# Optimization experiments

Hardware: AMD Instinct MI355X
Metric: run time of the kernel (lower is better)

## Reference

```python
import jax, jax.numpy as jnp
import numpy as np

N_TOKENS, E, H = 20000, 128, 512
B, T, L = 128, 512, 8


def setup_inputs() -> dict:
    key = jax.random.key(0)
    ks = jax.random.split(key, 9)
    s = 0.02
    return {
        "tokens": jax.random.randint(ks[0], (B, T, L), 0, N_TOKENS),
        "values": jax.random.uniform(ks[1], (B, T, L), dtype=jnp.float32),
        "emb": jax.random.normal(ks[2], (N_TOKENS, E), dtype=jnp.float32) * s,
        "W_ih": jax.random.normal(ks[3], (4 * H, E), dtype=jnp.float32) * s,
        "W_hh": jax.random.normal(ks[4], (4 * H, H), dtype=jnp.float32) * s,
        "b_ih": jnp.zeros((4 * H,), jnp.float32),
        "b_hh": jnp.zeros((4 * H,), jnp.float32),
        "W_out": jax.random.normal(ks[5], (1, H), dtype=jnp.float32) * s,
        "b_out": jnp.zeros((1,), jnp.float32),
    }


def reference(tokens, values, emb, W_ih, W_hh, b_ih, b_hh, W_out, b_out):
    # EmbedTimeseriesW: value-weighted sum of token embeddings per time bin
    e = emb[tokens]                                  # [B,T,L,E]
    x = jnp.einsum('btle,btl->bte', e, values)       # [B,T,E]
    x = jax.nn.relu(x)                               # ReLU (dropout p=0 -> identity)

    xT = jnp.swapaxes(x, 0, 1)                       # [T,B,E]
    b = b_ih + b_hh

    def step(carry, xt):
        h, c = carry
        gates = xt @ W_ih.T + h @ W_hh.T + b         # [B,4H]
        i, f, g, o = jnp.split(gates, 4, axis=-1)    # torch LSTM gate order
        c = jax.nn.sigmoid(f) * c + jax.nn.sigmoid(i) * jnp.tanh(g)
        h = jax.nn.sigmoid(o) * jnp.tanh(c)
        return (h, c), h

    h0 = jnp.zeros((x.shape[0], W_hh.shape[1]), x.dtype)
    (_, _), hs = jax.lax.scan(step, (h0, h0), xT)    # hs: [T,B,H]

    out = jnp.swapaxes(hs, 0, 1) @ W_out.T + b_out   # [B,T,1]
    return out.squeeze(-1)                           # [B,T]
```

## Files before the change

kernel.cpp:

```cpp
#include <hip/hip_runtime.h>
#include <hip/hip_bf16.h>

#define B_   128
#define T_   512
#define L_   8
#define E_   128
#define H_   512

#define NG_   8
#define WPG_  16
#define JW_   32
#define GSTR  132
#define HBUFB 131072
#define BARSA_OFF (3 * HBUFB)
#define FAST_BYTES (BARSA_OFF + NG_ * 64 * 4)
#define SPIN_MAX 4096

typedef __attribute__((ext_vector_type(8))) short s8v;
typedef __attribute__((ext_vector_type(4))) float f4v;
typedef __attribute__((ext_vector_type(4))) unsigned int u32x4;
typedef unsigned long long u64;
typedef unsigned int u32;

__device__ __forceinline__ float bf16u_to_f(unsigned short s) {
  union { unsigned u; float f; } c; c.u = ((unsigned)s) << 16; return c.f;
}
__device__ __forceinline__ u64 llc_load8(const void* p) {
  return __hip_atomic_load((const u64*)p, __ATOMIC_RELAXED, __HIP_MEMORY_SCOPE_AGENT);
}
__device__ __forceinline__ unsigned llc_load4(const unsigned* p) {
  return __hip_atomic_load(p, __ATOMIC_RELAXED, __HIP_MEMORY_SCOPE_AGENT);
}
__device__ __forceinline__ void llc_store4(unsigned* p, unsigned v) {
  __hip_atomic_store(p, v, __ATOMIC_RELAXED, __HIP_MEMORY_SCOPE_AGENT);
}
__device__ __forceinline__ float sigf(float x) {
  return __builtin_amdgcn_rcpf(1.f + __expf(-x));
}
__device__ __forceinline__ float tanh_f(float x) {
  return 1.f - 2.f * __builtin_amdgcn_rcpf(1.f + __expf(2.f * x));
}

__device__ __forceinline__ void buf_store_sc0(u32x4 srd, unsigned voff, unsigned v) {
  asm volatile("buffer_store_dword %0, %1, %2, 0 offen sc0"
               :: "v"(v), "v"(voff), "s"(srd) : "memory");
}
__device__ __forceinline__ unsigned buf_load_sc0(u32x4 srd, unsigned voff) {
  unsigned v;
  asm volatile("buffer_load_dword %0, %1, %2, 0 offen sc0\n\ts_waitcnt vmcnt(0)"
               : "=v"(v) : "v"(voff), "s"(srd) : "memory");
  return v;
}

__device__ __forceinline__ bool wait_flags_fast(u32x4 srd, unsigned polloff, unsigned tgt) {
  for (int it = 0; it < SPIN_MAX; ++it) {
    unsigned v = buf_load_sc0(srd, polloff);
    if (__all((int)(v >= tgt))) return true;
    __builtin_amdgcn_s_sleep(1);
  }
  return false;
}
__device__ __forceinline__ void wait_flags_slow(const u32* flags, unsigned tgt) {
  const u32* p = flags + (threadIdx.x & 63);
  while (!__all((int)(llc_load4(p) >= tgt))) __builtin_amdgcn_s_sleep(1);
}

__global__ void embed_kernel(const int* __restrict__ tokens,
                             const float* __restrict__ values,
                             const float* __restrict__ emb,
                             __hip_bfloat16* __restrict__ x_bf) {
  int idx = blockIdx.x * blockDim.x + threadIdx.x;
  int e  = idx & (E_ - 1);
  int bt = idx >> 7;
  int b  = bt >> 9;
  int t  = bt & (T_ - 1);
  const int*   tok = tokens + (size_t)bt * L_;
  const float* val = values + (size_t)bt * L_;
  float acc = 0.f;
#pragma unroll
  for (int l = 0; l < L_; ++l) acc += emb[(size_t)tok[l] * E_ + e] * val[l];
  acc = fmaxf(acc, 0.f);
  x_bf[((size_t)t * B_ + b) * E_ + e] = __float2bfloat16(acc);
}

__device__ __forceinline__ void fill_slab(u32x4* __restrict__ h_lds4, int mode,
                                          u32x4 srd, unsigned voffA,
                                          const u64* __restrict__ slow_src,
                                          int tid) {
  u32x4 c0, c1, c2, c3;
  if (mode == 0) {
    asm volatile(
        "buffer_load_dwordx4 %0, %4, %5, 0 offen sc0\n\t"
        "buffer_load_dwordx4 %1, %4, %5, 0 offen offset:16 sc0\n\t"
        "buffer_load_dwordx4 %2, %4, %5, 0 offen offset:32 sc0\n\t"
        "buffer_load_dwordx4 %3, %4, %5, 0 offen offset:48 sc0\n\t"
        "s_waitcnt vmcnt(0)"
        : "=&v"(c0), "=&v"(c1), "=&v"(c2), "=&v"(c3)
        : "v"(voffA), "s"(srd) : "memory");
  } else {
    u64 a, b;
    a = llc_load8(slow_src + 0); b = llc_load8(slow_src + 1);
    c0 = (u32x4){(u32)a, (u32)(a >> 32), (u32)b, (u32)(b >> 32)};
    a = llc_load8(slow_src + 2); b = llc_load8(slow_src + 3);
    c1 = (u32x4){(u32)a, (u32)(a >> 32), (u32)b, (u32)(b >> 32)};
    a = llc_load8(slow_src + 4); b = llc_load8(slow_src + 5);
    c2 = (u32x4){(u32)a, (u32)(a >> 32), (u32)b, (u32)(b >> 32)};
    a = llc_load8(slow_src + 6); b = llc_load8(slow_src + 7);
    c3 = (u32x4){(u32)a, (u32)(a >> 32), (u32)b, (u32)(b >> 32)};
  }
  const int row = tid >> 4;
  const int sw2 = row & 7;
  const int cb  = (tid & 15) * 4;
  u32x4* dst = h_lds4 + (size_t)row * 64;
  dst[(cb + 0) ^ sw2] = c0;
  dst[(cb + 1) ^ sw2] = c1;
  dst[(cb + 2) ^ sw2] = c2;
  dst[(cb + 3) ^ sw2] = c3;
}

__device__ __forceinline__ void out_dot_lds16(const u32x4* __restrict__ h_lds4,
                                              int t, int gid,
                                              const float* __restrict__ wout_s,
                                              float bout, float* __restrict__ out) {
  const int um = threadIdx.x >> 4;
  const int uj = threadIdx.x & 15;
  const u64* row = (const u64*)(h_lds4 + (size_t)um * 64);
  const float* wr = wout_s + uj * 32;
  float p = 0.f;
#pragma unroll
  for (int j = 0; j < 4; ++j) {
    int pc = ((uj * 4 + j) ^ (um & 7)) * 2;
    u64 qa = row[pc], qb = row[pc + 1];
    p += bf16u_to_f((unsigned short)(qa      )) * wr[j * 8 + 0];
    p += bf16u_to_f((unsigned short)(qa >> 16)) * wr[j * 8 + 1];
    p += bf16u_to_f((unsigned short)(qa >> 32)) * wr[j * 8 + 2];
    p += bf16u_to_f((unsigned short)(qa >> 48)) * wr[j * 8 + 3];
    p += bf16u_to_f((unsigned short)(qb      )) * wr[j * 8 + 4];
    p += bf16u_to_f((unsigned short)(qb >> 16)) * wr[j * 8 + 5];
    p += bf16u_to_f((unsigned short)(qb >> 32)) * wr[j * 8 + 6];
    p += bf16u_to_f((unsigned short)(qb >> 48)) * wr[j * 8 + 7];
  }
  p += __shfl_down(p, 8, 16);
  p += __shfl_down(p, 4, 16);
  p += __shfl_down(p, 2, 16);
  p += __shfl_down(p, 1, 16);
  if (uj == 0) out[(size_t)(gid * 16 + um) * T_ + t] = p + bout;
}

__global__ void __launch_bounds__(256, 1)
lstm_kernel(const float* __restrict__ W_ih, const float* __restrict__ W_hh,
            const float* __restrict__ b_ih, const float* __restrict__ b_hh,
            const float* __restrict__ W_out, const float* __restrict__ b_out,
            const __hip_bfloat16* __restrict__ x_bf,
            u64* __restrict__ h_slow,
            float* __restrict__ out,
            u32* __restrict__ barsB,
            u32* __restrict__ xcc_tab,
            char* __restrict__ fastbase) {
  __shared__ __align__(16) u32x4 h_lds4[16 * 64];
  __shared__ __align__(16) float gbuf[16][GSTR];
  __shared__ __align__(16) float bias_s[128];
  __shared__ float wout_s[H_];
  __shared__ int   cnt_same_s, bad_grp_s, mode_s;

  const int tid = threadIdx.x;
  const int wg  = blockIdx.x;
  const int gid = wg & (NG_ - 1);
  const int g   = wg >> 3;
  const int j0g = g * JW_;

  const int wv   = tid >> 6;
  const int lane = tid & 63;
  const int m16  = lane & 15;
  const int q    = lane >> 4;
  const int sw   = m16 & 7;

  u32x4 srd;
  {
    unsigned long long ba = (unsigned long long)fastbase;
    srd = (u32x4){(u32)ba, (u32)(ba >> 32) & 0xffffu, 0xffffffffu, 0x00020000u};
  }

  const unsigned xcc = (unsigned)__builtin_amdgcn_s_getreg(20 | (3 << 11));
  if (tid == 0) { cnt_same_s = 0; bad_grp_s = 0; llc_store4(xcc_tab + wg, xcc + 1u); }
  __syncthreads();
  if (tid < 128) {
    const u32* slot = xcc_tab + tid;
    unsigned v = llc_load4(slot);
    while (v == 0u) { __builtin_amdgcn_s_sleep(8); v = llc_load4(slot); }
    if (v == xcc + 1u) atomicAdd(&cnt_same_s, 1);
    else if ((tid & 7) == gid) bad_grp_s = 1;
  }
  __syncthreads();
  if (tid == 0) mode_s = ((bad_grp_s == 0) && (cnt_same_s <= 64)) ? 0 : 1;

  s8v bfrag[2][20];
#pragma unroll
  for (int nt = 0; nt < 2; ++nt) {
    const int r = wv * H_ + j0g + nt * 16 + m16;
    const float* wih_r = W_ih + (size_t)r * E_;
    const float* whh_r = W_hh + (size_t)r * H_;
#pragma unroll
    for (int ks = 0; ks < 20; ++ks) {
      s8v v;
#pragma unroll
      for (int i = 0; i < 8; ++i) {
        int k = ks * 32 + q * 8 + i;
        float w = (k < E_) ? wih_r[k] : whh_r[k - E_];
        __hip_bfloat16 hb = __float2bfloat16(w);
        v[i] = *(short*)&hb;
      }
      bfrag[nt][ks] = v;
    }
  }
  if (tid < 128) {
    int gt = tid >> 5, jl = tid & 31;
    int r = gt * H_ + j0g + jl;
    bias_s[tid] = b_ih[r] + b_hh[r];
  }
  if (g == 0) for (int i = tid; i < H_; i += 256) wout_s[i] = W_out[i];

  const int um = tid >> 4;
  const int jb = (tid & 15) * 2;
  const int ub = gid * 16 + um;
  float cst[2] = {0.f, 0.f};
  const float bout = b_out[0];
  u32* h_slow32 = (u32*)h_slow;
  u32* flagsB   = barsB + gid * 64;
  u32* myflagB  = flagsB + (g << 2) + wv;
  const unsigned hoffA_base  = (unsigned)(ub * 1024 + (g * 16 + (tid & 15)) * 4);
  const unsigned hslow_base  = (unsigned)(ub * 256 + g * 16 + (tid & 15));
  const unsigned flagAoff    = (unsigned)(BARSA_OFF + (gid * 64 + (g << 2) + wv) * 4);
  const unsigned polloff     = (unsigned)(BARSA_OFF + (gid * 64 + (tid & 63)) * 4);
  const unsigned filloffA    = (unsigned)((gid * 16 + (tid >> 4)) * 1024 + (tid & 15) * 64);
  const unsigned slab_u64off = (unsigned)(gid * 16 * 128 + tid * 8);

  int rp = 2, wp = 0;
  f4v acc[2];

  {
    const __hip_bfloat16* ax0 = x_bf + (size_t)(gid * 16 + m16) * E_ + q * 8;
    f4v z = {0.f, 0.f, 0.f, 0.f};
    acc[0] = z; acc[1] = z;
#pragma unroll
    for (int ks = 0; ks < 4; ++ks) {
      s8v a0 = *(const s8v*)(ax0 + ks * 32);
#pragma unroll
      for (int nt = 0; nt < 2; ++nt)
        acc[nt] = __builtin_amdgcn_mfma_f32_16x16x32_bf16(a0, bfrag[nt][ks], acc[nt], 0, 0, 0);
    }
  }
  __syncthreads();

  for (int t = 0; t < T_; ++t) {
    if (wv == 0) {
      int m0 = mode_s;
      bool got = false;
      if (m0 == 0) {
        got = wait_flags_fast(srd, polloff, (unsigned)t);
        if (!got && lane == 0) mode_s = 1;
      }
      if (!got) wait_flags_slow(flagsB, (unsigned)t);
    }
    __syncthreads();
    const int mode = mode_s;

    fill_slab(h_lds4, mode, srd, (unsigned)(rp * HBUFB) + filloffA,
              h_slow + (size_t)rp * 16384 + slab_u64off, tid);
    __syncthreads();

    {
      const s8v* arow = (const s8v*)(h_lds4 + (size_t)m16 * 64);
#pragma unroll
      for (int ks4 = 0; ks4 < 16; ++ks4) {
        s8v a0 = arow[(ks4 * 4 + q) ^ sw];
#pragma unroll
        for (int nt = 0; nt < 2; ++nt)
          acc[nt] = __builtin_amdgcn_mfma_f32_16x16x32_bf16(a0, bfrag[nt][4 + ks4], acc[nt], 0, 0, 0);
      }
    }

#pragma unroll
    for (int nt = 0; nt < 2; ++nt)
#pragma unroll
      for (int r = 0; r < 4; ++r)
        gbuf[q * 4 + r][wv * 32 + nt * 16 + m16] = acc[nt][r];
    __syncthreads();

    {
      const float* gr = &gbuf[um][0];
      float si0 = sigf(gr[jb]      + bias_s[jb]);
      float si1 = sigf(gr[jb + 1]  + bias_s[jb + 1]);
      float sf0 = sigf(gr[32 + jb] + bias_s[32 + jb]);
      float sf1 = sigf(gr[33 + jb] + bias_s[33 + jb]);
      float tg0 = tanh_f(gr[64 + jb] + bias_s[64 + jb]);
      float tg1 = tanh_f(gr[65 + jb] + bias_s[65 + jb]);
      float so0 = sigf(gr[96 + jb] + bias_s[96 + jb]);
      float so1 = sigf(gr[97 + jb] + bias_s[97 + jb]);
      cst[0] = sf0 * cst[0] + si0 * tg0;
      cst[1] = sf1 * cst[1] + si1 * tg1;
      float h0 = so0 * tanh_f(cst[0]);
      float h1 = so1 * tanh_f(cst[1]);
      __hip_bfloat16 hb0 = __float2bfloat16(h0);
      __hip_bfloat16 hb1 = __float2bfloat16(h1);
      u32 w = (u32)(*(unsigned short*)&hb0) | ((u32)(*(unsigned short*)&hb1) << 16);
      buf_store_sc0(srd, (unsigned)(wp * HBUFB) + hoffA_base, w);
      llc_store4(h_slow32 + (size_t)wp * 32768 + hslow_base, w);
      asm volatile("s_waitcnt vmcnt(1)" ::: "memory");
      if (lane == 0) buf_store_sc0(srd, flagAoff, (unsigned)(t + 1));
      asm volatile("s_waitcnt vmcnt(0)" ::: "memory");
      if (lane == 0) llc_store4(myflagB, (unsigned)(t + 1));
    }

    if (g == 0 && t > 0)
      out_dot_lds16(h_lds4, t - 1, gid, wout_s, bout, out);

    if (t + 1 < T_) {
      const __hip_bfloat16* xt = x_bf + (size_t)(t + 1) * B_ * E_;
      const __hip_bfloat16* ax0 = xt + (size_t)(gid * 16 + m16) * E_ + q * 8;
      f4v z = {0.f, 0.f, 0.f, 0.f};
      acc[0] = z; acc[1] = z;
#pragma unroll
      for (int ks = 0; ks < 4; ++ks) {
        s8v a0 = *(const s8v*)(ax0 + ks * 32);
#pragma unroll
        for (int nt = 0; nt < 2; ++nt)
          acc[nt] = __builtin_amdgcn_mfma_f32_16x16x32_bf16(a0, bfrag[nt][ks], acc[nt], 0, 0, 0);
      }
    }

    rp = wp; wp = (wp == 2) ? 0 : wp + 1;
  }

  if (g == 0) {
    if (wv == 0) {
      int m0 = mode_s;
      bool got = false;
      if (m0 == 0) {
        got = wait_flags_fast(srd, polloff, (unsigned)T_);
        if (!got && lane == 0) mode_s = 1;
      }
      if (!got) wait_flags_slow(flagsB, (unsigned)T_);
    }
    __syncthreads();
    fill_slab(h_lds4, mode_s, srd, (unsigned)(rp * HBUFB) + filloffA,
              h_slow + (size_t)rp * 16384 + slab_u64off, tid);
    __syncthreads();
    out_dot_lds16(h_lds4, T_ - 1, gid, wout_s, bout, out);
  }
}

extern "C" void kernel_launch(void* const* d_in, const int* in_sizes, int n_in,
                              void* d_out, int out_size, void* d_ws, size_t ws_size,
                              hipStream_t stream) {
  const int*   tokens = (const int*)d_in[0];
  const float* values = (const float*)d_in[1];
  const float* emb    = (const float*)d_in[2];
  const float* W_ih   = (const float*)d_in[3];
  const float* W_hh   = (const float*)d_in[4];
  const float* b_ih   = (const float*)d_in[5];
  const float* b_hh   = (const float*)d_in[6];
  const float* W_out  = (const float*)d_in[7];
  const float* b_out  = (const float*)d_in[8];
  float* out = (float*)d_out;

  char* ws = (char*)d_ws;
  __hip_bfloat16* x_bf = (__hip_bfloat16*)ws;
  char* p = ws + (size_t)T_ * B_ * E_ * 2;
  u64*  h_slow  = (u64*)p;
  u32*  barsB   = (u32*)(p + 3 * HBUFB);
  u32*  xcc_tab = (u32*)(p + 3 * HBUFB + 2048);
  char* fastbase = p + 3 * HBUFB + 2048 + 512;

  hipMemsetAsync(p, 0, (size_t)(3 * HBUFB + 2048 + 512) + FAST_BYTES, stream);

  embed_kernel<<<(B_ * T_ * E_) / 256, 256, 0, stream>>>(tokens, values, emb, x_bf);

  lstm_kernel<<<dim3(NG_ * WPG_), dim3(256), 0, stream>>>(
      W_ih, W_hh, b_ih, b_hh, W_out, b_out, x_bf, h_slow, out, barsB, xcc_tab,
      fastbase);
}
```

Measured before the change: 2.073 ms.

## Load recurrent h fragments directly into registers and drop per-step LDS staging barriers

Each wave now polls the cross-workgroup flags itself and loads its MFMA A-fragments of the previous hidden state straight from the shared global buffer into registers, replacing the cooperative LDS slab fill and its two block barriers per step. The gate buffer is double-buffered so only one __syncthreads remains per timestep, and the output dot product reads h from global memory instead of LDS. The slow-path flag store is moved after the next input projection, and the fast spin loop sleeps only every eighth poll. This trades redundant global loads (every wave loads the full row set) and more polling traffic for a shorter critical path per timestep. The fallback mode is now decided per wave rather than block-wide, which could let waves diverge in which buffer they read.

```diff
diff --git a/kernel.cpp b/kernel.cpp
--- a/kernel.cpp
+++ b/kernel.cpp
@@ -12,6 +12,8 @@
 #define JW_   32
 #define GSTR  132
 #define HBUFB 131072
+#define HSU32 32768
+#define HSU64 16384
 #define BARSA_OFF (3 * HBUFB)
 #define FAST_BYTES (BARSA_OFF + NG_ * 64 * 4)
 #define SPIN_MAX 4096
@@ -25,6 +27,9 @@
 __device__ __forceinline__ float bf16u_to_f(unsigned short s) {
   union { unsigned u; float f; } c; c.u = ((unsigned)s) << 16; return c.f;
 }
+__device__ __forceinline__ s8v as_s8v(u32x4 v) {
+  union { u32x4 u; s8v s; } c; c.u = v; return c.s;
+}
 __device__ __forceinline__ u64 llc_load8(const void* p) {
   return __hip_atomic_load((const u64*)p, __ATOMIC_RELAXED, __HIP_MEMORY_SCOPE_AGENT);
 }
@@ -56,7 +61,7 @@
   for (int it = 0; it < SPIN_MAX; ++it) {
     unsigned v = buf_load_sc0(srd, polloff);
     if (__all((int)(v >= tgt))) return true;
-    __builtin_amdgcn_s_sleep(1);
+    if ((it & 7) == 7) __builtin_amdgcn_s_sleep(1);
   }
   return false;
 }
@@ -83,12 +88,25 @@
   x_bf[((size_t)t * B_ + b) * E_ + e] = __float2bfloat16(acc);
 }
 
-__device__ __forceinline__ void fill_slab(u32x4* __restrict__ h_lds4, int mode,
-                                          u32x4 srd, unsigned voffA,
-                                          const u64* __restrict__ slow_src,
-                                          int tid) {
+__device__ __forceinline__ float mac8(u32x4 c, const float* wr, float p) {
+#pragma unroll
+  for (int i = 0; i < 4; ++i) {
+    p += bf16u_to_f((unsigned short)(c[i] & 0xffffu)) * wr[2 * i];
+    p += bf16u_to_f((unsigned short)(c[i] >> 16))     * wr[2 * i + 1];
+  }
+  return p;
+}
+
+__device__ __forceinline__ void out_dot_g(int mode, u32x4 srd, unsigned bufbyte,
+                                          const u64* __restrict__ slow_buf,
+                                          int t, int gid,
+                                          const float* __restrict__ wout_s,
+                                          float bout, float* __restrict__ out) {
+  const int um = threadIdx.x >> 4;
+  const int uj = threadIdx.x & 15;
   u32x4 c0, c1, c2, c3;
   if (mode == 0) {
+    unsigned voff = bufbyte + (unsigned)((gid * 16 + um) * 1024 + uj * 64);
     asm volatile(
         "buffer_load_dwordx4 %0, %4, %5, 0 offen sc0\n\t"
         "buffer_load_dwordx4 %1, %4, %5, 0 offen offset:16 sc0\n\t"
@@ -96,50 +114,25 @@
         "buffer_load_dwordx4 %3, %4, %5, 0 offen offset:48 sc0\n\t"
         "s_waitcnt vmcnt(0)"
         : "=&v"(c0), "=&v"(c1), "=&v"(c2), "=&v"(c3)
-        : "v"(voffA), "s"(srd) : "memory");
+        : "v"(voff), "s"(srd) : "memory");
   } else {
+    const u64* s = slow_buf + (size_t)(gid * 16 + um) * 128 + uj * 8;
     u64 a, b;
-    a = llc_load8(slow_src + 0); b = llc_load8(slow_src + 1);
+    a = llc_load8(s + 0); b = llc_load8(s + 1);
     c0 = (u32x4){(u32)a, (u32)(a >> 32), (u32)b, (u32)(b >> 32)};
-    a = llc_load8(slow_src + 2); b = llc_load8(slow_src + 3);
+    a = llc_load8(s + 2); b = llc_load8(s + 3);
     c1 = (u32x4){(u32)a, (u32)(a >> 32), (u32)b, (u32)(b >> 32)};
-    a = llc_load8(slow_src + 4); b = llc_load8(slow_src + 5);
+    a = llc_load8(s + 4); b = llc_load8(s + 5);
     c2 = (u32x4){(u32)a, (u32)(a >> 32), (u32)b, (u32)(b >> 32)};
-    a = llc_load8(slow_src + 6); b = llc_load8(slow_src + 7);
+    a = llc_load8(s + 6); b = llc_load8(s + 7);
     c3 = (u32x4){(u32)a, (u32)(a >> 32), (u32)b, (u32)(b >> 32)};
   }
-  const int row = tid >> 4;
-  const int sw2 = row & 7;
-  const int cb  = (tid & 15) * 4;
-  u32x4* dst = h_lds4 + (size_t)row * 64;
-  dst[(cb + 0) ^ sw2] = c0;
-  dst[(cb + 1) ^ sw2] = c1;
-  dst[(cb + 2) ^ sw2] = c2;
-  dst[(cb + 3) ^ sw2] = c3;
-}
-
-__device__ __forceinline__ void out_dot_lds16(const u32x4* __restrict__ h_lds4,
-                                              int t, int gid,
-                                              const float* __restrict__ wout_s,
-                                              float bout, float* __restrict__ out) {
-  const int um = threadIdx.x >> 4;
-  const int uj = threadIdx.x & 15;
-  const u64* row = (const u64*)(h_lds4 + (size_t)um * 64);
   const float* wr = wout_s + uj * 32;
   float p = 0.f;
-#pragma unroll
-  for (int j = 0; j < 4; ++j) {
-    int pc = ((uj * 4 + j) ^ (um & 7)) * 2;
-    u64 qa = row[pc], qb = row[pc + 1];
-    p += bf16u_to_f((unsigned short)(qa      )) * wr[j * 8 + 0];
-    p += bf16u_to_f((unsigned short)(qa >> 16)) * wr[j * 8 + 1];
-    p += bf16u_to_f((unsigned short)(qa >> 32)) * wr[j * 8 + 2];
-    p += bf16u_to_f((unsigned short)(qa >> 48)) * wr[j * 8 + 3];
-    p += bf16u_to_f((unsigned short)(qb      )) * wr[j * 8 + 4];
-    p += bf16u_to_f((unsigned short)(qb >> 16)) * wr[j * 8 + 5];
-    p += bf16u_to_f((unsigned short)(qb >> 32)) * wr[j * 8 + 6];
-    p += bf16u_to_f((unsigned short)(qb >> 48)) * wr[j * 8 + 7];
-  }
+  p = mac8(c0, wr + 0,  p);
+  p = mac8(c1, wr + 8,  p);
+  p = mac8(c2, wr + 16, p);
+  p = mac8(c3, wr + 24, p);
   p += __shfl_down(p, 8, 16);
   p += __shfl_down(p, 4, 16);
   p += __shfl_down(p, 2, 16);
@@ -157,8 +150,7 @@
             u32* __restrict__ barsB,
             u32* __restrict__ xcc_tab,
             char* __restrict__ fastbase) {
-  __shared__ __align__(16) u32x4 h_lds4[16 * 64];
-  __shared__ __align__(16) float gbuf[16][GSTR];
+  __shared__ __align__(16) float gbuf[2][16][GSTR];
   __shared__ __align__(16) float bias_s[128];
   __shared__ float wout_s[H_];
   __shared__ int   cnt_same_s, bad_grp_s, mode_s;
@@ -173,7 +165,6 @@
   const int lane = tid & 63;
   const int m16  = lane & 15;
   const int q    = lane >> 4;
-  const int sw   = m16 & 7;
 
   u32x4 srd;
   {
@@ -228,12 +219,12 @@
   u32* h_slow32 = (u32*)h_slow;
   u32* flagsB   = barsB + gid * 64;
   u32* myflagB  = flagsB + (g << 2) + wv;
-  const unsigned hoffA_base  = (unsigned)(ub * 1024 + (g * 16 + (tid & 15)) * 4);
-  const unsigned hslow_base  = (unsigned)(ub * 256 + g * 16 + (tid & 15));
-  const unsigned flagAoff    = (unsigned)(BARSA_OFF + (gid * 64 + (g << 2) + wv) * 4);
-  const unsigned polloff     = (unsigned)(BARSA_OFF + (gid * 64 + (tid & 63)) * 4);
-  const unsigned filloffA    = (unsigned)((gid * 16 + (tid >> 4)) * 1024 + (tid & 15) * 64);
-  const unsigned slab_u64off = (unsigned)(gid * 16 * 128 + tid * 8);
+  const unsigned hoffA_base = (unsigned)(ub * 1024 + (g * 16 + (tid & 15)) * 4);
+  const unsigned hslow_base = (unsigned)(ub * 256 + g * 16 + (tid & 15));
+  const unsigned flagAoff   = (unsigned)(BARSA_OFF + (gid * 64 + (g << 2) + wv) * 4);
+  const unsigned polloff    = (unsigned)(BARSA_OFF + (gid * 64 + lane) * 4);
+  const unsigned arow_byte  = (unsigned)((gid * 16 + m16) * 1024 + q * 16);
+  const size_t   arow_u64   = (size_t)(gid * 16 + m16) * 128 + q * 2;
 
   int rp = 2, wp = 0;
   f4v acc[2];
@@ -251,44 +242,74 @@
     }
   }
   __syncthreads();
+  int mode = mode_s;
 
   for (int t = 0; t < T_; ++t) {
-    if (wv == 0) {
-      int m0 = mode_s;
+    {
       bool got = false;
-      if (m0 == 0) {
+      if (mode == 0) {
         got = wait_flags_fast(srd, polloff, (unsigned)t);
-        if (!got && lane == 0) mode_s = 1;
+        if (!got) mode = 1;
       }
       if (!got) wait_flags_slow(flagsB, (unsigned)t);
     }
+
+    u32x4 af[16];
+    if (mode == 0) {
+      const unsigned abase = (unsigned)(rp * HBUFB) + arow_byte;
+      asm volatile(
+          "buffer_load_dwordx4 %0, %8, %9, 0 offen sc0\n\t"
+          "buffer_load_dwordx4 %1, %8, %9, 0 offen offset:64 sc0\n\t"
+          "buffer_load_dwordx4 %2, %8, %9, 0 offen offset:128 sc0\n\t"
+          "buffer_load_dwordx4 %3, %8, %9, 0 offen offset:192 sc0\n\t"
+          "buffer_load_dwordx4 %4, %8, %9, 0 offen offset:256 sc0\n\t"
+          "buffer_load_dwordx4 %5, %8, %9, 0 offen offset:320 sc0\n\t"
+          "buffer_load_dwordx4 %6, %8, %9, 0 offen offset:384 sc0\n\t"
+          "buffer_load_dwordx4 %7, %8, %9, 0 offen offset:448 sc0"
+          : "=&v"(af[0]), "=&v"(af[1]), "=&v"(af[2]), "=&v"(af[3]),
+            "=&v"(af[4]), "=&v"(af[5]), "=&v"(af[6]), "=&v"(af[7])
+          : "v"(abase), "s"(srd) : "memory");
+      asm volatile(
+          "buffer_load_dwordx4 %0, %8, %9, 0 offen offset:512 sc0\n\t"
+          "buffer_load_dwordx4 %1, %8, %9, 0 offen offset:576 sc0\n\t"
+          "buffer_load_dwordx4 %2, %8, %9, 0 offen offset:640 sc0\n\t"
+          "buffer_load_dwordx4 %3, %8, %9, 0 offen offset:704 sc0\n\t"
+          "buffer_load_dwordx4 %4, %8, %9, 0 offen offset:768 sc0\n\t"
+          "buffer_load_dwordx4 %5, %8, %9, 0 offen offset:832 sc0\n\t"
+          "buffer_load_dwordx4 %6, %8, %9, 0 offen offset:896 sc0\n\t"
+          "buffer_load_dwordx4 %7, %8, %9, 0 offen offset:960 sc0\n\t"
+          "s_waitcnt vmcnt(0)"
+          : "=&v"(af[8]),  "=&v"(af[9]),  "=&v"(af[10]), "=&v"(af[11]),
+            "=&v"(af[12]), "=&v"(af[13]), "=&v"(af[14]), "=&v"(af[15])
+          : "v"(abase), "s"(srd) : "memory");
+    } else {
+      const u64* s = h_slow + (size_t)rp * HSU64 + arow_u64;
+#pragma unroll
+      for (int k = 0; k < 16; ++k) {
+        u64 a = llc_load8(s + k * 8);
+        u64 b = llc_load8(s + k * 8 + 1);
+        af[k] = (u32x4){(u32)a, (u32)(a >> 32), (u32)b, (u32)(b >> 32)};
+      }
+    }
+
+#pragma unroll
+    for (int k = 0; k < 16; ++k) {
+      s8v a0 = as_s8v(af[k]);
+#pragma unroll
+      for (int nt = 0; nt < 2; ++nt)
+        acc[nt] = __builtin_amdgcn_mfma_f32_16x16x32_bf16(a0, bfrag[nt][4 + k], acc[nt], 0, 0, 0);
+    }
+
+    const int cur = t & 1;
+#pragma unroll
+    for (int nt = 0; nt < 2; ++nt)
+#pragma unroll
+      for (int r = 0; r < 4; ++r)
+        gbuf[cur][q * 4 + r][wv * 32 + nt * 16 + m16] = acc[nt][r];
     __syncthreads();
-    const int mode = mode_s;
-
-    fill_slab(h_lds4, mode, srd, (unsigned)(rp * HBUFB) + filloffA,
-              h_slow + (size_t)rp * 16384 + slab_u64off, tid);
-    __syncthreads();
 
     {
-      const s8v* arow = (const s8v*)(h_lds4 + (size_t)m16 * 64);
-#pragma unroll
-      for (int ks4 = 0; ks4 < 16; ++ks4) {
-        s8v a0 = arow[(ks4 * 4 + q) ^ sw];
-#pragma unroll
-        for (int nt = 0; nt < 2; ++nt)
-          acc[nt] = __builtin_amdgcn_mfma_f32_16x16x32_bf16(a0, bfrag[nt][4 + ks4], acc[nt], 0, 0, 0);
-      }
-    }
-
-#pragma unroll
-    for (int nt = 0; nt < 2; ++nt)
-#pragma unroll
-      for (int r = 0; r < 4; ++r)
-        gbuf[q * 4 + r][wv * 32 + nt * 16 + m16] = acc[nt][r];
-    __syncthreads();
-
-    {
-      const float* gr = &gbuf[um][0];
+      const float* gr = &gbuf[cur][um][0];
       float si0 = sigf(gr[jb]      + bias_s[jb]);
       float si1 = sigf(gr[jb + 1]  + bias_s[jb + 1]);
       float sf0 = sigf(gr[32 + jb] + bias_s[32 + jb]);
@@ -305,15 +326,14 @@
       __hip_bfloat16 hb1 = __float2bfloat16(h1);
       u32 w = (u32)(*(unsigned short*)&hb0) | ((u32)(*(unsigned short*)&hb1) << 16);
       buf_store_sc0(srd, (unsigned)(wp * HBUFB) + hoffA_base, w);
-      llc_store4(h_slow32 + (size_t)wp * 32768 + hslow_base, w);
+      llc_store4(h_slow32 + (size_t)wp * HSU32 + hslow_base, w);
       asm volatile("s_waitcnt vmcnt(1)" ::: "memory");
       if (lane == 0) buf_store_sc0(srd, flagAoff, (unsigned)(t + 1));
-      asm volatile("s_waitcnt vmcnt(0)" ::: "memory");
-      if (lane == 0) llc_store4(myflagB, (unsigned)(t + 1));
     }
 
     if (g == 0 && t > 0)
-      out_dot_lds16(h_lds4, t - 1, gid, wout_s, bout, out);
+      out_dot_g(mode, srd, (unsigned)(rp * HBUFB), h_slow + (size_t)rp * HSU64,
+                t - 1, gid, wout_s, bout, out);
 
     if (t + 1 < T_) {
       const __hip_bfloat16* xt = x_bf + (size_t)(t + 1) * B_ * E_;
@@ -329,24 +349,21 @@
       }
     }
 
+    asm volatile("s_waitcnt vmcnt(0)" ::: "memory");
+    if (lane == 0) llc_store4(myflagB, (unsigned)(t + 1));
+
     rp = wp; wp = (wp == 2) ? 0 : wp + 1;
   }
 
   if (g == 0) {
-    if (wv == 0) {
-      int m0 = mode_s;
-      bool got = false;
-      if (m0 == 0) {
-        got = wait_flags_fast(srd, polloff, (unsigned)T_);
-        if (!got && lane == 0) mode_s = 1;
-      }
-      if (!got) wait_flags_slow(flagsB, (unsigned)T_);
-    }
-    __syncthreads();
-    fill_slab(h_lds4, mode_s, srd, (unsigned)(rp * HBUFB) + filloffA,
-              h_slow + (size_t)rp * 16384 + slab_u64off, tid);
-    __syncthreads();
-    out_dot_lds16(h_lds4, T_ - 1, gid, wout_s, bout, out);
+    bool got = false;
+    if (mode == 0) {
+      got = wait_flags_fast(srd, polloff, (unsigned)T_);
+      if (!got) mode = 1;
+    }
+    if (!got) wait_flags_slow(flagsB, (unsigned)T_);
+    out_dot_g(mode, srd, (unsigned)(rp * HBUFB), h_slow + (size_t)rp * HSU64,
+              T_ - 1, gid, wout_s, bout, out);
   }
 }
 
```

After: 5.395 ms. 160% more time.

## Remap MFMA weight columns so LSTM gates combine in registers, dropping LDS gate buffer

Applied to the files above, without the earlier changes.

Reorders the W_ih/W_hh rows loaded into each wave's MFMA B fragments so that every wave holds all four gates (i,f,g,o) for 8 hidden units. Gate values are then paired with a lane shuffle instead of being written to an LDS gate buffer and read back after a block-wide barrier. That removes one __syncthreads and the LDS round trip per timestep on the serial recurrence path. The slow-path flag store is also deferred until after the next step's input MFMA, so its memory wait overlaps with compute. In exchange, half the lanes now issue the h stores with a different addressing pattern, and the wait-count logic becomes more delicate.

```diff
diff --git a/kernel.cpp b/kernel.cpp
--- a/kernel.cpp
+++ b/kernel.cpp
@@ -10,8 +10,9 @@
 #define NG_   8
 #define WPG_  16
 #define JW_   32
-#define GSTR  132
 #define HBUFB 131072
+#define HSU32 32768
+#define HSU64 16384
 #define BARSA_OFF (3 * HBUFB)
 #define FAST_BYTES (BARSA_OFF + NG_ * 64 * 4)
 #define SPIN_MAX 4096
@@ -158,8 +159,6 @@
             u32* __restrict__ xcc_tab,
             char* __restrict__ fastbase) {
   __shared__ __align__(16) u32x4 h_lds4[16 * 64];
-  __shared__ __align__(16) float gbuf[16][GSTR];
-  __shared__ __align__(16) float bias_s[128];
   __shared__ float wout_s[H_];
   __shared__ int   cnt_same_s, bad_grp_s, mode_s;
 
@@ -174,6 +173,7 @@
   const int m16  = lane & 15;
   const int q    = lane >> 4;
   const int sw   = m16 & 7;
+  const int jl   = m16 & 7;
 
   u32x4 srd;
   {
@@ -197,7 +197,8 @@
   s8v bfrag[2][20];
 #pragma unroll
   for (int nt = 0; nt < 2; ++nt) {
-    const int r = wv * H_ + j0g + nt * 16 + m16;
+    const int gt = (nt == 0) ? ((m16 < 8) ? 0 : 1) : ((m16 < 8) ? 2 : 3);
+    const int r  = gt * H_ + j0g + wv * 8 + jl;
     const float* wih_r = W_ih + (size_t)r * E_;
     const float* whh_r = W_hh + (size_t)r * H_;
 #pragma unroll
@@ -213,26 +214,24 @@
       bfrag[nt][ks] = v;
     }
   }
-  if (tid < 128) {
-    int gt = tid >> 5, jl = tid & 31;
-    int r = gt * H_ + j0g + jl;
-    bias_s[tid] = b_ih[r] + b_hh[r];
-  }
+  const int ju = j0g + wv * 8 + jl;
+  const float bi_r = b_ih[0 * H_ + ju] + b_hh[0 * H_ + ju];
+  const float bf_r = b_ih[1 * H_ + ju] + b_hh[1 * H_ + ju];
+  const float bg_r = b_ih[2 * H_ + ju] + b_hh[2 * H_ + ju];
+  const float bo_r = b_ih[3 * H_ + ju] + b_hh[3 * H_ + ju];
   if (g == 0) for (int i = tid; i < H_; i += 256) wout_s[i] = W_out[i];
 
-  const int um = tid >> 4;
-  const int jb = (tid & 15) * 2;
-  const int ub = gid * 16 + um;
+  const bool low    = (m16 < 8);
+  const int  rowadd = low ? 0 : 2;
+  const int  up     = j0g + wv * 8 + (jl & ~1);
   float cst[2] = {0.f, 0.f};
   const float bout = b_out[0];
   u32* h_slow32 = (u32*)h_slow;
   u32* flagsB   = barsB + gid * 64;
   u32* myflagB  = flagsB + (g << 2) + wv;
-  const unsigned hoffA_base  = (unsigned)(ub * 1024 + (g * 16 + (tid & 15)) * 4);
-  const unsigned hslow_base  = (unsigned)(ub * 256 + g * 16 + (tid & 15));
-  const unsigned flagAoff    = (unsigned)(BARSA_OFF + (gid * 64 + (g << 2) + wv) * 4);
-  const unsigned polloff     = (unsigned)(BARSA_OFF + (gid * 64 + (tid & 63)) * 4);
-  const unsigned filloffA    = (unsigned)((gid * 16 + (tid >> 4)) * 1024 + (tid & 15) * 64);
+  const unsigned flagAoff   = (unsigned)(BARSA_OFF + (gid * 64 + (g << 2) + wv) * 4);
+  const unsigned polloff    = (unsigned)(BARSA_OFF + (gid * 64 + lane) * 4);
+  const unsigned filloffA   = (unsigned)((gid * 16 + (tid >> 4)) * 1024 + (tid & 15) * 64);
   const unsigned slab_u64off = (unsigned)(gid * 16 * 128 + tid * 8);
 
   int rp = 2, wp = 0;
@@ -266,7 +265,7 @@
     const int mode = mode_s;
 
     fill_slab(h_lds4, mode, srd, (unsigned)(rp * HBUFB) + filloffA,
-              h_slow + (size_t)rp * 16384 + slab_u64off, tid);
+              h_slow + (size_t)rp * HSU64 + slab_u64off, tid);
     __syncthreads();
 
     {
@@ -280,36 +279,49 @@
       }
     }
 
-#pragma unroll
-    for (int nt = 0; nt < 2; ++nt)
-#pragma unroll
-      for (int r = 0; r < 4; ++r)
-        gbuf[q * 4 + r][wv * 32 + nt * 16 + m16] = acc[nt][r];
-    __syncthreads();
-
     {
-      const float* gr = &gbuf[um][0];
-      float si0 = sigf(gr[jb]      + bias_s[jb]);
-      float si1 = sigf(gr[jb + 1]  + bias_s[jb + 1]);
-      float sf0 = sigf(gr[32 + jb] + bias_s[32 + jb]);
-      float sf1 = sigf(gr[33 + jb] + bias_s[33 + jb]);
-      float tg0 = tanh_f(gr[64 + jb] + bias_s[64 + jb]);
-      float tg1 = tanh_f(gr[65 + jb] + bias_s[65 + jb]);
-      float so0 = sigf(gr[96 + jb] + bias_s[96 + jb]);
-      float so1 = sigf(gr[97 + jb] + bias_s[97 + jb]);
-      cst[0] = sf0 * cst[0] + si0 * tg0;
-      cst[1] = sf1 * cst[1] + si1 * tg1;
-      float h0 = so0 * tanh_f(cst[0]);
-      float h1 = so1 * tanh_f(cst[1]);
-      __hip_bfloat16 hb0 = __float2bfloat16(h0);
-      __hip_bfloat16 hb1 = __float2bfloat16(h1);
-      u32 w = (u32)(*(unsigned short*)&hb0) | ((u32)(*(unsigned short*)&hb1) << 16);
-      buf_store_sc0(srd, (unsigned)(wp * HBUFB) + hoffA_base, w);
-      llc_store4(h_slow32 + (size_t)wp * 32768 + hslow_base, w);
-      asm volatile("s_waitcnt vmcnt(1)" ::: "memory");
+      f4v ya, yb;
+#pragma unroll
+      for (int i = 0; i < 4; ++i) {
+        ya[i] = __shfl_xor(acc[0][i], 8);
+        yb[i] = __shfl_xor(acc[1][i], 8);
+      }
+      u32 wpk[2];
+#pragma unroll
+      for (int rr = 0; rr < 2; ++rr) {
+        const int ri = rowadd + rr;
+        float iv = low ? acc[0][ri] : ya[ri];
+        float fv = low ? ya[ri]     : acc[0][ri];
+        float gv = low ? acc[1][ri] : yb[ri];
+        float ov = low ? yb[ri]     : acc[1][ri];
+        float ii = sigf(iv + bi_r);
+        float ff = sigf(fv + bf_r);
+        float gg = tanh_f(gv + bg_r);
+        float oo = sigf(ov + bo_r);
+        cst[rr] = ff * cst[rr] + ii * gg;
+        float h = oo * tanh_f(cst[rr]);
+        __hip_bfloat16 hb = __float2bfloat16(h);
+        unsigned short hu = *(unsigned short*)&hb;
+        unsigned short pu = (unsigned short)__shfl_xor((int)hu, 1);
+        wpk[rr] = ((jl & 1) == 0) ? ((u32)hu | ((u32)pu << 16))
+                                  : ((u32)pu | ((u32)hu << 16));
+      }
+      if ((jl & 1) == 0) {
+#pragma unroll
+        for (int rr = 0; rr < 2; ++rr) {
+          const int brow = q * 4 + rowadd + rr;
+          buf_store_sc0(srd, (unsigned)(wp * HBUFB)
+                             + (unsigned)((gid * 16 + brow) * 1024 + up * 2), wpk[rr]);
+        }
+#pragma unroll
+        for (int rr = 0; rr < 2; ++rr) {
+          const int brow = q * 4 + rowadd + rr;
+          llc_store4(h_slow32 + (size_t)wp * HSU32
+                              + (gid * 16 + brow) * 256 + (up >> 1), wpk[rr]);
+        }
+      }
+      asm volatile("s_waitcnt vmcnt(2)" ::: "memory");
       if (lane == 0) buf_store_sc0(srd, flagAoff, (unsigned)(t + 1));
-      asm volatile("s_waitcnt vmcnt(0)" ::: "memory");
-      if (lane == 0) llc_store4(myflagB, (unsigned)(t + 1));
     }
 
     if (g == 0 && t > 0)
@@ -328,6 +340,9 @@
           acc[nt] = __builtin_amdgcn_mfma_f32_16x16x32_bf16(a0, bfrag[nt][ks], acc[nt], 0, 0, 0);
       }
     }
+
+    asm volatile("s_waitcnt vmcnt(0)" ::: "memory");
+    if (lane == 0) llc_store4(myflagB, (unsigned)(t + 1));
 
     rp = wp; wp = (wp == 2) ? 0 : wp + 1;
   }
@@ -344,7 +359,7 @@
     }
     __syncthreads();
     fill_slab(h_lds4, mode_s, srd, (unsigned)(rp * HBUFB) + filloffA,
-              h_slow + (size_t)rp * 16384 + slab_u64off, tid);
+              h_slow + (size_t)rp * HSU64 + slab_u64off, tid);
     __syncthreads();
     out_dot_lds16(h_lds4, T_ - 1, gid, wout_s, bout, out);
   }
```

Result: slower. 3.110 ms (+50.1%).

## Double LSTM block width to 512 threads, one MFMA tile per wave

Applied to the files above, without the earlier changes.

Each workgroup now runs 8 waves instead of 4, and each wave owns one 16-column gate tile rather than two. This halves the per-wave MFMA chain and register use in the serial recurrent step. The recurrent K-loop is split across two accumulators to expose MFMA ILP. Gate math becomes one hidden unit per thread, with a shuffle to pack bf16 pairs. The flag arrays double to one flag per wave, and the slow-path flag store is deferred until after the next input projection so it overlaps. The trade-off is more flags to poll per barrier and more waves to synchronise with __syncthreads each timestep.

```diff
diff --git a/kernel.cpp b/kernel.cpp
--- a/kernel.cpp
+++ b/kernel.cpp
@@ -12,13 +12,17 @@
 #define JW_   32
 #define GSTR  132
 #define HBUFB 131072
+#define HSU32 32768
+#define HSU64 16384
 #define BARSA_OFF (3 * HBUFB)
-#define FAST_BYTES (BARSA_OFF + NG_ * 64 * 4)
+#define NFLG  128
+#define FAST_BYTES (BARSA_OFF + NG_ * NFLG * 4)
 #define SPIN_MAX 4096
 
 typedef __attribute__((ext_vector_type(8))) short s8v;
 typedef __attribute__((ext_vector_type(4))) float f4v;
 typedef __attribute__((ext_vector_type(4))) unsigned int u32x4;
+typedef __attribute__((ext_vector_type(2))) unsigned int u32x2;
 typedef unsigned long long u64;
 typedef unsigned int u32;
 
@@ -45,24 +49,32 @@
   asm volatile("buffer_store_dword %0, %1, %2, 0 offen sc0"
                :: "v"(v), "v"(voff), "s"(srd) : "memory");
 }
-__device__ __forceinline__ unsigned buf_load_sc0(u32x4 srd, unsigned voff) {
-  unsigned v;
-  asm volatile("buffer_load_dword %0, %1, %2, 0 offen sc0\n\ts_waitcnt vmcnt(0)"
+__device__ __forceinline__ void buf_store_sc0_x1(u32x4 srd, unsigned voff, unsigned v) {
+  asm volatile("buffer_store_dword %0, %1, %2, 0 offen sc0"
+               :: "v"(v), "v"(voff), "s"(srd) : "memory");
+}
+__device__ __forceinline__ u32x2 buf_load8_sc0(u32x4 srd, unsigned voff) {
+  u32x2 v;
+  asm volatile("buffer_load_dwordx2 %0, %1, %2, 0 offen sc0\n\ts_waitcnt vmcnt(0)"
                : "=v"(v) : "v"(voff), "s"(srd) : "memory");
   return v;
 }
 
 __device__ __forceinline__ bool wait_flags_fast(u32x4 srd, unsigned polloff, unsigned tgt) {
   for (int it = 0; it < SPIN_MAX; ++it) {
-    unsigned v = buf_load_sc0(srd, polloff);
-    if (__all((int)(v >= tgt))) return true;
+    u32x2 v = buf_load8_sc0(srd, polloff);
+    if (__all((int)(v[0] >= tgt && v[1] >= tgt))) return true;
     __builtin_amdgcn_s_sleep(1);
   }
   return false;
 }
 __device__ __forceinline__ void wait_flags_slow(const u32* flags, unsigned tgt) {
-  const u32* p = flags + (threadIdx.x & 63);
-  while (!__all((int)(llc_load4(p) >= tgt))) __builtin_amdgcn_s_sleep(1);
+  const u32* p = flags + (threadIdx.x & 63) * 2;
+  for (;;) {
+    u64 v = llc_load8(p);
+    if (__all((int)((u32)v >= tgt && (u32)(v >> 32) >= tgt))) return;
+    __builtin_amdgcn_s_sleep(1);
+  }
 }
 
 __global__ void embed_kernel(const int* __restrict__ tokens,
@@ -87,15 +99,13 @@
                                           u32x4 srd, unsigned voffA,
                                           const u64* __restrict__ slow_src,
                                           int tid) {
-  u32x4 c0, c1, c2, c3;
+  u32x4 c0, c1;
   if (mode == 0) {
     asm volatile(
-        "buffer_load_dwordx4 %0, %4, %5, 0 offen sc0\n\t"
-        "buffer_load_dwordx4 %1, %4, %5, 0 offen offset:16 sc0\n\t"
-        "buffer_load_dwordx4 %2, %4, %5, 0 offen offset:32 sc0\n\t"
-        "buffer_load_dwordx4 %3, %4, %5, 0 offen offset:48 sc0\n\t"
+        "buffer_load_dwordx4 %0, %2, %3, 0 offen sc0\n\t"
+        "buffer_load_dwordx4 %1, %2, %3, 0 offen offset:16 sc0\n\t"
         "s_waitcnt vmcnt(0)"
-        : "=&v"(c0), "=&v"(c1), "=&v"(c2), "=&v"(c3)
+        : "=&v"(c0), "=&v"(c1)
         : "v"(voffA), "s"(srd) : "memory");
   } else {
     u64 a, b;
@@ -103,25 +113,20 @@
     c0 = (u32x4){(u32)a, (u32)(a >> 32), (u32)b, (u32)(b >> 32)};
     a = llc_load8(slow_src + 2); b = llc_load8(slow_src + 3);
     c1 = (u32x4){(u32)a, (u32)(a >> 32), (u32)b, (u32)(b >> 32)};
-    a = llc_load8(slow_src + 4); b = llc_load8(slow_src + 5);
-    c2 = (u32x4){(u32)a, (u32)(a >> 32), (u32)b, (u32)(b >> 32)};
-    a = llc_load8(slow_src + 6); b = llc_load8(slow_src + 7);
-    c3 = (u32x4){(u32)a, (u32)(a >> 32), (u32)b, (u32)(b >> 32)};
-  }
-  const int row = tid >> 4;
+  }
+  const int row = tid >> 5;
   const int sw2 = row & 7;
-  const int cb  = (tid & 15) * 4;
+  const int cb  = (tid & 31) * 2;
   u32x4* dst = h_lds4 + (size_t)row * 64;
   dst[(cb + 0) ^ sw2] = c0;
   dst[(cb + 1) ^ sw2] = c1;
-  dst[(cb + 2) ^ sw2] = c2;
-  dst[(cb + 3) ^ sw2] = c3;
 }
 
 __device__ __forceinline__ void out_dot_lds16(const u32x4* __restrict__ h_lds4,
                                               int t, int gid,
                                               const float* __restrict__ wout_s,
                                               float bout, float* __restrict__ out) {
+  if (threadIdx.x >= 256) return;
   const int um = threadIdx.x >> 4;
   const int uj = threadIdx.x & 15;
   const u64* row = (const u64*)(h_lds4 + (size_t)um * 64);
@@ -147,7 +152,7 @@
   if (uj == 0) out[(size_t)(gid * 16 + um) * T_ + t] = p + bout;
 }
 
-__global__ void __launch_bounds__(256, 1)
+__global__ void __launch_bounds__(512, 1)
 lstm_kernel(const float* __restrict__ W_ih, const float* __restrict__ W_hh,
             const float* __restrict__ b_ih, const float* __restrict__ b_hh,
             const float* __restrict__ W_out, const float* __restrict__ b_out,
@@ -169,7 +174,7 @@
   const int g   = wg >> 3;
   const int j0g = g * JW_;
 
-  const int wv   = tid >> 6;
+  const int w    = tid >> 6;
   const int lane = tid & 63;
   const int m16  = lane & 15;
   const int q    = lane >> 4;
@@ -194,10 +199,10 @@
   __syncthreads();
   if (tid == 0) mode_s = ((bad_grp_s == 0) && (cnt_same_s <= 64)) ? 0 : 1;
 
-  s8v bfrag[2][20];
-#pragma unroll
-  for (int nt = 0; nt < 2; ++nt) {
-    const int r = wv * H_ + j0g + nt * 16 + m16;
+  s8v bfrag[20];
+  {
+    const int gt = w & 3;
+    const int r  = gt * H_ + j0g + (w >> 2) * 16 + m16;
     const float* wih_r = W_ih + (size_t)r * E_;
     const float* whh_r = W_hh + (size_t)r * H_;
 #pragma unroll
@@ -206,11 +211,11 @@
 #pragma unroll
       for (int i = 0; i < 8; ++i) {
         int k = ks * 32 + q * 8 + i;
-        float w = (k < E_) ? wih_r[k] : whh_r[k - E_];
-        __hip_bfloat16 hb = __float2bfloat16(w);
+        float ww = (k < E_) ? wih_r[k] : whh_r[k - E_];
+        __hip_bfloat16 hb = __float2bfloat16(ww);
         v[i] = *(short*)&hb;
       }
-      bfrag[nt][ks] = v;
+      bfrag[ks] = v;
     }
   }
   if (tid < 128) {
@@ -218,42 +223,39 @@
     int r = gt * H_ + j0g + jl;
     bias_s[tid] = b_ih[r] + b_hh[r];
   }
-  if (g == 0) for (int i = tid; i < H_; i += 256) wout_s[i] = W_out[i];
-
-  const int um = tid >> 4;
-  const int jb = (tid & 15) * 2;
+  if (g == 0) for (int i = tid; i < H_; i += 512) wout_s[i] = W_out[i];
+
+  const int um = tid >> 5;
+  const int j  = tid & 31;
   const int ub = gid * 16 + um;
-  float cst[2] = {0.f, 0.f};
+  float cst = 0.f;
   const float bout = b_out[0];
   u32* h_slow32 = (u32*)h_slow;
-  u32* flagsB   = barsB + gid * 64;
-  u32* myflagB  = flagsB + (g << 2) + wv;
-  const unsigned hoffA_base  = (unsigned)(ub * 1024 + (g * 16 + (tid & 15)) * 4);
-  const unsigned hslow_base  = (unsigned)(ub * 256 + g * 16 + (tid & 15));
-  const unsigned flagAoff    = (unsigned)(BARSA_OFF + (gid * 64 + (g << 2) + wv) * 4);
-  const unsigned polloff     = (unsigned)(BARSA_OFF + (gid * 64 + (tid & 63)) * 4);
-  const unsigned filloffA    = (unsigned)((gid * 16 + (tid >> 4)) * 1024 + (tid & 15) * 64);
-  const unsigned slab_u64off = (unsigned)(gid * 16 * 128 + tid * 8);
+  u32* flagsB   = barsB + gid * NFLG;
+  u32* myflagB  = flagsB + g * 8 + w;
+  const unsigned flagAoff   = (unsigned)(BARSA_OFF + (gid * NFLG + g * 8 + w) * 4);
+  const unsigned polloff    = (unsigned)(BARSA_OFF + (gid * NFLG + lane * 2) * 4);
+  const unsigned filloffA   = (unsigned)((gid * 16 + (tid >> 5)) * 1024 + (tid & 31) * 32);
+  const unsigned slab_u64off = (unsigned)(gid * 16 * 128 + tid * 4);
+  const unsigned hstoreA = (unsigned)(ub * 1024 + (j0g + j) * 2);
+  const unsigned hstoreS = (unsigned)(ub * 256 + ((j0g + j) >> 1));
 
   int rp = 2, wp = 0;
-  f4v acc[2];
+  f4v acc;
 
   {
     const __hip_bfloat16* ax0 = x_bf + (size_t)(gid * 16 + m16) * E_ + q * 8;
-    f4v z = {0.f, 0.f, 0.f, 0.f};
-    acc[0] = z; acc[1] = z;
+    acc = (f4v){0.f, 0.f, 0.f, 0.f};
 #pragma unroll
     for (int ks = 0; ks < 4; ++ks) {
       s8v a0 = *(const s8v*)(ax0 + ks * 32);
-#pragma unroll
-      for (int nt = 0; nt < 2; ++nt)
-        acc[nt] = __builtin_amdgcn_mfma_f32_16x16x32_bf16(a0, bfrag[nt][ks], acc[nt], 0, 0, 0);
+      acc = __builtin_amdgcn_mfma_f32_16x16x32_bf16(a0, bfrag[ks], acc, 0, 0, 0);
     }
   }
   __syncthreads();
 
   for (int t = 0; t < T_; ++t) {
-    if (wv == 0) {
+    if (w == 0) {
       int m0 = mode_s;
       bool got = false;
       if (m0 == 0) {
@@ -266,50 +268,48 @@
     const int mode = mode_s;
 
     fill_slab(h_lds4, mode, srd, (unsigned)(rp * HBUFB) + filloffA,
-              h_slow + (size_t)rp * 16384 + slab_u64off, tid);
+              h_slow + (size_t)rp * HSU64 + slab_u64off, tid);
     __syncthreads();
 
     {
       const s8v* arow = (const s8v*)(h_lds4 + (size_t)m16 * 64);
-#pragma unroll
-      for (int ks4 = 0; ks4 < 16; ++ks4) {
+      f4v acc2 = (f4v){0.f, 0.f, 0.f, 0.f};
+#pragma unroll
+      for (int ks4 = 0; ks4 < 16; ks4 += 2) {
         s8v a0 = arow[(ks4 * 4 + q) ^ sw];
-#pragma unroll
-        for (int nt = 0; nt < 2; ++nt)
-          acc[nt] = __builtin_amdgcn_mfma_f32_16x16x32_bf16(a0, bfrag[nt][4 + ks4], acc[nt], 0, 0, 0);
-      }
-    }
-
-#pragma unroll
-    for (int nt = 0; nt < 2; ++nt)
+        s8v a1 = arow[((ks4 + 1) * 4 + q) ^ sw];
+        acc  = __builtin_amdgcn_mfma_f32_16x16x32_bf16(a0, bfrag[4 + ks4], acc, 0, 0, 0);
+        acc2 = __builtin_amdgcn_mfma_f32_16x16x32_bf16(a1, bfrag[5 + ks4], acc2, 0, 0, 0);
+      }
+      acc[0] += acc2[0]; acc[1] += acc2[1]; acc[2] += acc2[2]; acc[3] += acc2[3];
+    }
+
+    {
+      const int col = (w & 3) * 32 + (w >> 2) * 16 + m16;
 #pragma unroll
       for (int r = 0; r < 4; ++r)
-        gbuf[q * 4 + r][wv * 32 + nt * 16 + m16] = acc[nt][r];
+        gbuf[q * 4 + r][col] = acc[r];
+    }
     __syncthreads();
 
     {
       const float* gr = &gbuf[um][0];
-      float si0 = sigf(gr[jb]      + bias_s[jb]);
-      float si1 = sigf(gr[jb + 1]  + bias_s[jb + 1]);
-      float sf0 = sigf(gr[32 + jb] + bias_s[32 + jb]);
-      float sf1 = sigf(gr[33 + jb] + bias_s[33 + jb]);
-      float tg0 = tanh_f(gr[64 + jb] + bias_s[64 + jb]);
-      float tg1 = tanh_f(gr[65 + jb] + bias_s[65 + jb]);
-      float so0 = sigf(gr[96 + jb] + bias_s[96 + jb]);
-      float so1 = sigf(gr[97 + jb] + bias_s[97 + jb]);
-      cst[0] = sf0 * cst[0] + si0 * tg0;
-      cst[1] = sf1 * cst[1] + si1 * tg1;
-      float h0 = so0 * tanh_f(cst[0]);
-      float h1 = so1 * tanh_f(cst[1]);
-      __hip_bfloat16 hb0 = __float2bfloat16(h0);
-      __hip_bfloat16 hb1 = __float2bfloat16(h1);
-      u32 w = (u32)(*(unsigned short*)&hb0) | ((u32)(*(unsigned short*)&hb1) << 16);
-      buf_store_sc0(srd, (unsigned)(wp * HBUFB) + hoffA_base, w);
-      llc_store4(h_slow32 + (size_t)wp * 32768 + hslow_base, w);
+      float ii = sigf(gr[j]      + bias_s[j]);
+      float ff = sigf(gr[32 + j] + bias_s[32 + j]);
+      float gg = tanh_f(gr[64 + j] + bias_s[64 + j]);
+      float oo = sigf(gr[96 + j] + bias_s[96 + j]);
+      cst = ff * cst + ii * gg;
+      float h = oo * tanh_f(cst);
+      __hip_bfloat16 hb = __float2bfloat16(h);
+      unsigned short hu = *(unsigned short*)&hb;
+      unsigned short pu = (unsigned short)__shfl_xor((int)hu, 1);
+      if ((j & 1) == 0) {
+        u32 wv = (u32)hu | ((u32)pu << 16);
+        buf_store_sc0(srd, (unsigned)(wp * HBUFB) + hstoreA, wv);
+        llc_store4(h_slow32 + (size_t)wp * HSU32 + hstoreS, wv);
+      }
       asm volatile("s_waitcnt vmcnt(1)" ::: "memory");
-      if (lane == 0) buf_store_sc0(srd, flagAoff, (unsigned)(t + 1));
-      asm volatile("s_waitcnt vmcnt(0)" ::: "memory");
-      if (lane == 0) llc_store4(myflagB, (unsigned)(t + 1));
+      if (lane == 0) buf_store_sc0_x1(srd, flagAoff, (unsigned)(t + 1));
     }
 
     if (g == 0 && t > 0)
@@ -318,22 +318,22 @@
     if (t + 1 < T_) {
       const __hip_bfloat16* xt = x_bf + (size_t)(t + 1) * B_ * E_;
       const __hip_bfloat16* ax0 = xt + (size_t)(gid * 16 + m16) * E_ + q * 8;
-      f4v z = {0.f, 0.f, 0.f, 0.f};
-      acc[0] = z; acc[1] = z;
+      acc = (f4v){0.f, 0.f, 0.f, 0.f};
 #pragma unroll
       for (int ks = 0; ks < 4; ++ks) {
         s8v a0 = *(const s8v*)(ax0 + ks * 32);
-#pragma unroll
-        for (int nt = 0; nt < 2; ++nt)
-          acc[nt] = __builtin_amdgcn_mfma_f32_16x16x32_bf16(a0, bfrag[nt][ks], acc[nt], 0, 0, 0);
-      }
-    }
+        acc = __builtin_amdgcn_mfma_f32_16x16x32_bf16(a0, bfrag[ks], acc, 0, 0, 0);
+      }
+    }
+
+    asm volatile("s_waitcnt vmcnt(0)" ::: "memory");
+    if (lane == 0) llc_store4(myflagB, (unsigned)(t + 1));
 
     rp = wp; wp = (wp == 2) ? 0 : wp + 1;
   }
 
   if (g == 0) {
-    if (wv == 0) {
+    if (w == 0) {
       int m0 = mode_s;
       bool got = false;
       if (m0 == 0) {
@@ -344,7 +344,7 @@
     }
     __syncthreads();
     fill_slab(h_lds4, mode_s, srd, (unsigned)(rp * HBUFB) + filloffA,
-              h_slow + (size_t)rp * 16384 + slab_u64off, tid);
+              h_slow + (size_t)rp * HSU64 + slab_u64off, tid);
     __syncthreads();
     out_dot_lds16(h_lds4, T_ - 1, gid, wout_s, bout, out);
   }
@@ -369,14 +369,14 @@
   char* p = ws + (size_t)T_ * B_ * E_ * 2;
   u64*  h_slow  = (u64*)p;
   u32*  barsB   = (u32*)(p + 3 * HBUFB);
-  u32*  xcc_tab = (u32*)(p + 3 * HBUFB + 2048);
-  char* fastbase = p + 3 * HBUFB + 2048 + 512;
-
-  hipMemsetAsync(p, 0, (size_t)(3 * HBUFB + 2048 + 512) + FAST_BYTES, stream);
+  u32*  xcc_tab = (u32*)(p + 3 * HBUFB + 4096);
+  char* fastbase = p + 3 * HBUFB + 4096 + 512;
+
+  hipMemsetAsync(p, 0, (size_t)(3 * HBUFB + 4096 + 512) + FAST_BYTES, stream);
 
   embed_kernel<<<(B_ * T_ * E_) / 256, 256, 0, stream>>>(tokens, values, emb, x_bf);
 
-  lstm_kernel<<<dim3(NG_ * WPG_), dim3(256), 0, stream>>>(
+  lstm_kernel<<<dim3(NG_ * WPG_), dim3(512), 0, stream>>>(
       W_ih, W_hh, b_ih, b_hh, W_out, b_out, x_bf, h_slow, out, barsB, xcc_tab,
       fastbase);
 }
```

Measured after the change: 3.348 ms. 61.6% more time.
